# Kernel tuning notes

Measured on AMD Instinct MI355X. Metric: run time of the kernel, lower is better.

Reference implementation:

```python
import jax, jax.numpy as jnp
import numpy as np

V, E, S, B, N = 100000, 300, 1024, 64, 5
H = [512, 256, 128]

def setup_inputs() -> dict:
    key = jax.random.key(0)
    ks = jax.random.split(key, 10)
    x = jax.random.randint(ks[0], (B, S), 0, V, dtype=jnp.int32)
    # lengths must be >= n for valid n-gram counts (original assumes this)
    lengths = jax.random.randint(ks[1], (B,), N, S + 1, dtype=jnp.int32)
    sc = lambda f: 1.0 / np.sqrt(f)
    table = jax.random.normal(ks[2], (V, E), dtype=jnp.float32)
    W_slide = jax.random.uniform(ks[3], (N * E, H[0]), jnp.float32, -sc(N * E), sc(N * E))
    b_slide = jax.random.uniform(ks[4], (H[0],), jnp.float32, -sc(N * E), sc(N * E))
    W1 = jax.random.uniform(ks[5], (H[0], H[1]), jnp.float32, -sc(H[0]), sc(H[0]))
    b1 = jax.random.uniform(ks[6], (H[1],), jnp.float32, -sc(H[0]), sc(H[0]))
    W2 = jax.random.uniform(ks[7], (H[1], H[2]), jnp.float32, -sc(H[1]), sc(H[1]))
    b2 = jax.random.uniform(ks[8], (H[2],), jnp.float32, -sc(H[1]), sc(H[1]))
    return {"x": x, "lengths": lengths, "table": table, "W_slide": W_slide,
            "b_slide": b_slide, "W1": W1, "b1": b1, "W2": W2, "b2": b2}

def reference(x, lengths, table, W_slide, b_slide, W1, b1, W2, b2):
    n = N
    Wn = S - (n - 1)  # number of sliding windows per sequence
    emb = table[x]  # [B, S, E]
    # gather sliding windows: [B, Wn, n, E] -> [B, Wn, n*E]
    idx = jnp.arange(Wn)[:, None] + jnp.arange(n)[None, :]
    win = emb[:, idx].reshape(B, Wn, n * E)
    h = win @ W_slide + b_slide              # [B, Wn, H0]
    h = jax.nn.relu(h @ W1 + b1)             # [B, Wn, H1]
    h = jax.nn.relu(h @ W2 + b2)             # [B, Wn, H2]
    # ragged mean over valid n-gram positions per sample
    valid = (lengths - (n - 1)).astype(h.dtype)           # [B]
    mask = (jnp.arange(Wn)[None, :] < (lengths - (n - 1))[:, None]).astype(h.dtype)
    pooled = jnp.einsum('bwh,bw->bh', h, mask) / valid[:, None]
    return pooled
```

## Files before the change

kernel.cpp:

```cpp
#include <hip/hip_runtime.h>

#define B_N    64
#define S_LEN  1024
#define EMB    300
#define EMB_P  304
#define NGRAM  5
#define WPAD   1024
#define MTOT   (B_N * WPAD)
#define K1P    1536
#define H0     512
#define H1D    256
#define H2D    128
#define NK1    (K1P / 32)
#define NSTEP1 (K1P / 64)

#define GATHER_BLOCKS ((MTOT * (EMB_P / 4)) / 256)
#define WPREP_THREADS (H0 * K1P + H1D * H0 + H2D * H1D)
#define WPREP_BLOCKS  ((WPREP_THREADS + 255) / 256)

typedef _Float16 half8 __attribute__((ext_vector_type(8)));
typedef float  floatx4 __attribute__((ext_vector_type(4)));

typedef const __attribute__((address_space(1))) void* gptr_t;
typedef __attribute__((address_space(3))) void* sptr_t;

__device__ __forceinline__ void gload16(const void* g, void* s) {
  __builtin_amdgcn_global_load_lds((gptr_t)g, (sptr_t)s, 16, 0, 0);
}

__global__ void prep_kernel(const int* __restrict__ x,
                            const int* __restrict__ lengths,
                            const float* __restrict__ table,
                            _Float16* __restrict__ emb,
                            float* __restrict__ out,
                            const float* __restrict__ Ws,
                            const float* __restrict__ W1,
                            const float* __restrict__ W2,
                            _Float16* __restrict__ Bf1,
                            _Float16* __restrict__ Bf2,
                            _Float16* __restrict__ Bf3) {
  const int bid = blockIdx.x;
  if (bid < GATHER_BLOCKS) {
    if (bid < 32) out[bid * 256 + threadIdx.x] = 0.0f;
    const int CH = EMB_P / 4;
    int tid = bid * 256 + threadIdx.x;
    int tok = tid / CH;
    int c   = tid - tok * CH;
    int valid = lengths[tok >> 10] - (NGRAM - 1);
    int limit = ((valid + 127) & ~127) + 4;
    if ((tok & 1023) >= limit) return;
    int e   = c << 2;
    _Float16 h0, h1, h2, h3;
    if (e < EMB) {
      float4 v = *(const float4*)(table + (size_t)x[tok] * EMB + e);
      h0 = (_Float16)v.x; h1 = (_Float16)v.y; h2 = (_Float16)v.z; h3 = (_Float16)v.w;
    } else {
      h0 = h1 = h2 = h3 = (_Float16)0.0f;
    }
    union { float2 f2; _Float16 h[4]; } u;
    u.h[0] = h0; u.h[1] = h1; u.h[2] = h2; u.h[3] = h3;
    *(float2*)(emb + (size_t)tok * EMB_P + e) = u.f2;
  } else {
    int tid = (bid - GATHER_BLOCKS) * 256 + threadIdx.x;
    const int NS = H0 * K1P;
    const int N1 = H1D * H0;
    const int N2 = H2D * H1D;
    if (tid < NS) {
      int n = tid & 511, k = tid >> 9;
      float v = 0.0f;
      if (k < NGRAM * EMB_P) {
        int tn = k / EMB_P, e = k - tn * EMB_P;
        if (e < EMB) v = Ws[(size_t)(tn * EMB + e) * H0 + n];
      }
      int idx = ((((n >> 4) * NK1 + (k >> 5)) << 6) + (((k >> 3) & 3) << 4) + (n & 15)) * 8 + (k & 7);
      Bf1[idx] = (_Float16)v;
    } else if (tid < NS + N1) {
      int t = tid - NS;
      int n = t & 255, k = t >> 8;
      float v = W1[(size_t)k * H1D + n];
      int idx = ((((n >> 4) * 16 + (k >> 5)) << 6) + (((k >> 3) & 3) << 4) + (n & 15)) * 8 + (k & 7);
      Bf2[idx] = (_Float16)v;
    } else if (tid < NS + N1 + N2) {
      int t = tid - (NS + N1);
      int n = t & 127, k = t >> 7;
      float v = W2[(size_t)k * H2D + n];
      int idx = ((((n >> 4) * 8 + (k >> 5)) << 6) + (((k >> 3) & 3) << 4) + (n & 15)) * 8 + (k & 7);
      Bf3[idx] = (_Float16)v;
    }
  }
}

__global__ __launch_bounds__(256, 3)
void gemm1(const _Float16* __restrict__ A, const _Float16* __restrict__ Bf,
           const float* __restrict__ bias, _Float16* __restrict__ Cf,
           const int* __restrict__ lengths) {
  __shared__ _Float16 sA[2][128 * 64];

  const int tid  = threadIdx.x;
  const int wave = tid >> 6, lane = tid & 63;
  const int wr   = wave >> 1, wc = wave & 1;
  const int quad = lane >> 4, l16 = lane & 15;

  const int perX = gridDim.x >> 3;
  const int L  = (blockIdx.x & 7) * perX + (blockIdx.x >> 3);
  const int mt = L >> 2, nt = L & 3;
  if (((mt & 7) << 7) >= lengths[mt >> 3] - (NGRAM - 1)) return;
  const long mBase = (long)mt << 7;
  const int  nBase = nt << 7;

  const int srow0  = (wave << 3) + (lane >> 3);
  const int schunk = lane & 7;
  const _Float16* aG[4];
  int sOff[4];
#pragma unroll
  for (int p = 0; p < 4; p++) {
    int row = (p << 5) + srow0;
    int c   = schunk ^ (row & 7);
    aG[p]   = A + (mBase + row) * EMB_P + (c << 3);
    sOff[p] = (row << 6) + (schunk << 3);
  }

  const _Float16* bG[4];
#pragma unroll
  for (int j = 0; j < 4; j++)
    bG[j] = Bf + (((size_t)((nBase >> 4) + (wc << 2) + j) * NK1) << 9) + (lane << 3);

  int aOff[2][4];
#pragma unroll
  for (int s = 0; s < 2; s++)
#pragma unroll
    for (int i = 0; i < 4; i++) {
      int r    = (wr << 6) + (i << 4) + l16;
      int slot = ((s << 2) + quad) ^ (l16 & 7);
      aOff[s][i] = (r << 6) + (slot << 3);
    }

  floatx4 acc[4][4] = {};

#pragma unroll
  for (int p = 0; p < 4; p++) gload16(aG[p], &sA[0][sOff[p]]);
  half8 bCur[2][4], bNxt[2][4];
#pragma unroll
  for (int s = 0; s < 2; s++)
#pragma unroll
    for (int j = 0; j < 4; j++)
      bCur[s][j] = *(const half8*)(bG[j] + ((size_t)s << 9));

#pragma unroll 2
  for (int kk = 0; kk < NSTEP1; kk++) {
    const int cur = kk & 1;
    __syncthreads();
    if (kk + 1 < NSTEP1) {
      const int ko = (kk + 1) << 6;
#pragma unroll
      for (int p = 0; p < 4; p++) gload16(aG[p] + ko, &sA[cur ^ 1][sOff[p]]);
#pragma unroll
      for (int s = 0; s < 2; s++)
#pragma unroll
        for (int j = 0; j < 4; j++)
          bNxt[s][j] = *(const half8*)(bG[j] + (size_t)((((kk + 1) << 1) + s) << 9));
    }
#pragma unroll
    for (int s = 0; s < 2; s++) {
      half8 aFr[4];
#pragma unroll
      for (int i = 0; i < 4; i++)
        aFr[i] = *(const half8*)(&sA[cur][aOff[s][i]]);
#pragma unroll
      for (int i = 0; i < 4; i++)
#pragma unroll
        for (int j = 0; j < 4; j++)
          acc[i][j] = __builtin_amdgcn_mfma_f32_16x16x32_f16(aFr[i], bCur[s][j], acc[i][j], 0, 0, 0);
    }
#pragma unroll
    for (int s = 0; s < 2; s++)
#pragma unroll
      for (int j = 0; j < 4; j++)
        bCur[s][j] = bNxt[s][j];
  }

  __syncthreads();
  _Float16* cs = &sA[0][0];
#pragma unroll
  for (int j = 0; j < 4; j++) {
    int cl = (wc << 6) + (j << 4) + l16;
    float bv = bias[nBase + cl];
    int ksl = cl >> 5;
    int sub_hi = ((cl >> 3) & 3) << 4;
    int c7 = cl & 7;
#pragma unroll
    for (int i = 0; i < 4; i++) {
      int m16l = (wr << 2) + i;
#pragma unroll
      for (int r = 0; r < 4; r++) {
        int ml = (quad << 2) + r;
        cs[(((m16l << 2) + ksl) << 9) + ((sub_hi + ml) << 3) + c7] =
            (_Float16)(acc[i][j][r] + bv);
      }
    }
  }
  __syncthreads();
#pragma unroll
  for (int it = 0; it < 8; it++) {
    int cid = (it << 2) + wave;
    int m16l = cid >> 2, ksl = cid & 3;
    size_t g = ((size_t)(((mt << 3) + m16l) * 16 + (nt << 2) + ksl) << 9) + (lane << 3);
    *(half8*)(Cf + g) = *(const half8*)(cs + (cid << 9) + (lane << 3));
  }
}

__global__ __launch_bounds__(256, 2)
void gemm23(const _Float16* __restrict__ Af, const _Float16* __restrict__ B2,
            const _Float16* __restrict__ B3, const float* __restrict__ bias1,
            const float* __restrict__ bias2, float* __restrict__ out,
            const int* __restrict__ lengths) {
  __shared__ _Float16 sH[32768];
  __shared__ float red[2][128];

  const int tid  = threadIdx.x;
  const int wave = tid >> 6, lane = tid & 63;
  const int wr   = wave >> 1, wc = wave & 1;
  const int quad = lane >> 4, l16 = lane & 15;
  const int mt = blockIdx.x;

  const int b = mt >> 3;
  const int validw = lengths[b] - (NGRAM - 1);
  if (((mt & 7) << 7) >= validw) return;

  const _Float16* aR[4];
#pragma unroll
  for (int i = 0; i < 4; i++)
    aR[i] = Af + (((size_t)((mt << 3) + (wr << 2) + i) * 16) << 9) + (lane << 3);
  const _Float16* bR[8];
#pragma unroll
  for (int j = 0; j < 8; j++)
    bR[j] = B2 + (((size_t)((wc << 3) + j) * 16) << 9) + (lane << 3);

  floatx4 acc2[4][8] = {};
#pragma unroll 2
  for (int kk = 0; kk < 16; kk++) {
    const size_t ko = (size_t)kk << 9;
    half8 aF[4], bF[8];
#pragma unroll
    for (int i = 0; i < 4; i++) aF[i] = *(const half8*)(aR[i] + ko);
#pragma unroll
    for (int j = 0; j < 8; j++) bF[j] = *(const half8*)(bR[j] + ko);
#pragma unroll
    for (int i = 0; i < 4; i++)
#pragma unroll
      for (int j = 0; j < 8; j++)
        acc2[i][j] = __builtin_amdgcn_mfma_f32_16x16x32_f16(aF[i], bF[j], acc2[i][j], 0, 0, 0);
  }

#pragma unroll
  for (int j = 0; j < 8; j++) {
    int n = (wc << 7) + (j << 4) + l16;
    float bv = bias1[n];
    int ks = n >> 5;
    int sub_hi = ((n >> 3) & 3) << 4;
    int c7 = n & 7;
#pragma unroll
    for (int i = 0; i < 4; i++) {
      int m16l = (wr << 2) + i;
#pragma unroll
      for (int r = 0; r < 4; r++) {
        int ml = (quad << 2) + r;
        sH[(((m16l << 3) + ks) << 9) + ((sub_hi + ml) << 3) + c7] =
            (_Float16)fmaxf(acc2[i][j][r] + bv, 0.0f);
      }
    }
  }
  __syncthreads();

  const _Float16* b3R[4];
#pragma unroll
  for (int j = 0; j < 4; j++)
    b3R[j] = B3 + (((size_t)((wc << 2) + j) * 8) << 9) + (lane << 3);

  floatx4 acc3[4][4] = {};
#pragma unroll
  for (int ks = 0; ks < 8; ks++) {
    half8 aF[4], bF[4];
#pragma unroll
    for (int i = 0; i < 4; i++)
      aF[i] = *(const half8*)(sH + (((((wr << 2) + i) << 3) + ks) << 9) + (lane << 3));
#pragma unroll
    for (int j = 0; j < 4; j++) bF[j] = *(const half8*)(b3R[j] + ((size_t)ks << 9));
#pragma unroll
    for (int i = 0; i < 4; i++)
#pragma unroll
      for (int j = 0; j < 4; j++)
        acc3[i][j] = __builtin_amdgcn_mfma_f32_16x16x32_f16(aF[i], bF[j], acc3[i][j], 0, 0, 0);
  }

  float inv = 1.0f / (float)validw;
  int wBase = ((mt & 7) << 7) + (wr << 6);
#pragma unroll
  for (int j = 0; j < 4; j++) {
    int col = (wc << 6) + (j << 4) + l16;
    float bv = bias2[col];
    float p = 0.0f;
#pragma unroll
    for (int i = 0; i < 4; i++) {
#pragma unroll
      for (int r = 0; r < 4; r++) {
        int w = wBase + (i << 4) + (quad << 2) + r;
        float v = fmaxf(acc3[i][j][r] + bv, 0.0f);
        p += (w < validw) ? v : 0.0f;
      }
    }
    p *= inv;
    p += __shfl_xor(p, 16, 64);
    p += __shfl_xor(p, 32, 64);
    if (quad == 0) red[wr][col] = p;
  }
  __syncthreads();
  if (tid < 128) atomicAdd(out + b * H2D + tid, red[0][tid] + red[1][tid]);
}

extern "C" void kernel_launch(void* const* d_in, const int* in_sizes, int n_in,
                              void* d_out, int out_size, void* d_ws, size_t ws_size,
                              hipStream_t stream) {
  const int*   x       = (const int*)d_in[0];
  const int*   lengths = (const int*)d_in[1];
  const float* table   = (const float*)d_in[2];
  const float* W_slide = (const float*)d_in[3];
  const float* b_slide = (const float*)d_in[4];
  const float* W1      = (const float*)d_in[5];
  const float* b1      = (const float*)d_in[6];
  const float* W2      = (const float*)d_in[7];
  const float* b2      = (const float*)d_in[8];
  float* out = (float*)d_out;

  _Float16* ws  = (_Float16*)d_ws;
  _Float16* emb = ws;
  _Float16* Bf1 = emb + (size_t)MTOT * EMB_P + 4096;
  _Float16* Bf2 = Bf1 + (size_t)H0 * K1P;
  _Float16* Bf3 = Bf2 + (size_t)H1D * H0;
  _Float16* h1f = Bf3 + (size_t)H2D * H1D;

  prep_kernel<<<GATHER_BLOCKS + WPREP_BLOCKS, 256, 0, stream>>>(
      x, lengths, table, emb, out, W_slide, W1, W2, Bf1, Bf2, Bf3);
  gemm1<<<(MTOT / 128) * (H0 / 128), 256, 0, stream>>>(emb, Bf1, b_slide, h1f, lengths);
  gemm23<<<MTOT / 128, 256, 0, stream>>>(h1f, Bf2, Bf3, b1, b2, out, lengths);
}
```

Measured before the change: 292.3 us.

## Compact live M-tiles into a work list and widen gather stores

Adds a prep block that builds a compacted list of live 128-row tiles from the sequence lengths. gemm1 and gemm23 index that list, so live work is spread evenly across XCDs instead of leaving idle early-exit blocks scattered through the grid. The embedding gather now handles eight halves per thread with 16-byte stores. gemm23's layer-2 loop is also rewritten to double-buffer its global fragment loads in registers, which raises register pressure.

```diff
diff --git a/kernel.cpp b/kernel.cpp
--- a/kernel.cpp
+++ b/kernel.cpp
@@ -14,7 +14,7 @@
 #define NK1    (K1P / 32)
 #define NSTEP1 (K1P / 64)
 
-#define GATHER_BLOCKS ((MTOT * (EMB_P / 4)) / 256)
+#define GATHER_BLOCKS ((MTOT * 38) / 256)
 #define WPREP_THREADS (H0 * K1P + H1D * H0 + H2D * H1D)
 #define WPREP_BLOCKS  ((WPREP_THREADS + 255) / 256)
 
@@ -38,29 +38,30 @@
                             const float* __restrict__ W2,
                             _Float16* __restrict__ Bf1,
                             _Float16* __restrict__ Bf2,
-                            _Float16* __restrict__ Bf3) {
+                            _Float16* __restrict__ Bf3,
+                            int* __restrict__ meta) {
+  __shared__ int sN[64], sP[65];
   const int bid = blockIdx.x;
   if (bid < GATHER_BLOCKS) {
     if (bid < 32) out[bid * 256 + threadIdx.x] = 0.0f;
-    const int CH = EMB_P / 4;
     int tid = bid * 256 + threadIdx.x;
-    int tok = tid / CH;
-    int c   = tid - tok * CH;
+    int tok = tid / 38;
+    int c   = tid - tok * 38;
     int valid = lengths[tok >> 10] - (NGRAM - 1);
-    int limit = ((valid + 127) & ~127) + 4;
+    int limit = ((valid + 127) & ~127) + (NGRAM - 1);
     if ((tok & 1023) >= limit) return;
-    int e   = c << 2;
-    _Float16 h0, h1, h2, h3;
-    if (e < EMB) {
-      float4 v = *(const float4*)(table + (size_t)x[tok] * EMB + e);
-      h0 = (_Float16)v.x; h1 = (_Float16)v.y; h2 = (_Float16)v.z; h3 = (_Float16)v.w;
-    } else {
-      h0 = h1 = h2 = h3 = (_Float16)0.0f;
-    }
-    union { float2 f2; _Float16 h[4]; } u;
-    u.h[0] = h0; u.h[1] = h1; u.h[2] = h2; u.h[3] = h3;
-    *(float2*)(emb + (size_t)tok * EMB_P + e) = u.f2;
-  } else {
+    int e = c << 3;
+    const float* row = table + (size_t)x[tok] * EMB + e;
+    float4 v0 = *(const float4*)row;
+    float4 v1 = make_float4(0.0f, 0.0f, 0.0f, 0.0f);
+    if (e + 4 < EMB) v1 = *(const float4*)(row + 4);
+    union { half8 h8; _Float16 h[8]; } u;
+    u.h[0] = (_Float16)v0.x; u.h[1] = (_Float16)v0.y;
+    u.h[2] = (_Float16)v0.z; u.h[3] = (_Float16)v0.w;
+    u.h[4] = (_Float16)v1.x; u.h[5] = (_Float16)v1.y;
+    u.h[6] = (_Float16)v1.z; u.h[7] = (_Float16)v1.w;
+    *(half8*)(emb + (size_t)tok * EMB_P + e) = u.h8;
+  } else if (bid < GATHER_BLOCKS + WPREP_BLOCKS) {
     int tid = (bid - GATHER_BLOCKS) * 256 + threadIdx.x;
     const int NS = H0 * K1P;
     const int N1 = H1D * H0;
@@ -87,24 +88,42 @@
       int idx = ((((n >> 4) * 8 + (k >> 5)) << 6) + (((k >> 3) & 3) << 4) + (n & 15)) * 8 + (k & 7);
       Bf3[idx] = (_Float16)v;
     }
+  } else {
+    int t = threadIdx.x;
+    if (t < 64) sN[t] = (lengths[t] - (NGRAM - 1) + 127) >> 7;
+    __syncthreads();
+    if (t == 0) {
+      int s = 0;
+      for (int i = 0; i < 64; i++) { sP[i] = s; s += sN[i]; }
+      sP[64] = s;
+      meta[0] = s;
+    }
+    __syncthreads();
+    if (t < 64) {
+      int base = sP[t], n = sN[t];
+      for (int i = 0; i < n; i++) meta[8 + base + i] = (t << 3) + i;
+    }
   }
 }
 
 __global__ __launch_bounds__(256, 3)
 void gemm1(const _Float16* __restrict__ A, const _Float16* __restrict__ Bf,
            const float* __restrict__ bias, _Float16* __restrict__ Cf,
-           const int* __restrict__ lengths) {
+           const int* __restrict__ meta) {
   __shared__ _Float16 sA[2][128 * 64];
+
+  const int nLive4 = meta[0] << 2;
+  const int xcd = blockIdx.x & 7, bi = blockIdx.x >> 3;
+  const int q = nLive4 >> 3, r = nLive4 & 7;
+  if (bi >= q + (xcd < r ? 1 : 0)) return;
+  const int L = xcd * q + (xcd < r ? xcd : r) + bi;
+  const int mt = meta[8 + (L >> 2)], nt = L & 3;
 
   const int tid  = threadIdx.x;
   const int wave = tid >> 6, lane = tid & 63;
   const int wr   = wave >> 1, wc = wave & 1;
   const int quad = lane >> 4, l16 = lane & 15;
 
-  const int perX = gridDim.x >> 3;
-  const int L  = (blockIdx.x & 7) * perX + (blockIdx.x >> 3);
-  const int mt = L >> 2, nt = L & 3;
-  if (((mt & 7) << 7) >= lengths[mt >> 3] - (NGRAM - 1)) return;
   const long mBase = (long)mt << 7;
   const int  nBase = nt << 7;
 
@@ -130,9 +149,9 @@
   for (int s = 0; s < 2; s++)
 #pragma unroll
     for (int i = 0; i < 4; i++) {
-      int r    = (wr << 6) + (i << 4) + l16;
+      int rr   = (wr << 6) + (i << 4) + l16;
       int slot = ((s << 2) + quad) ^ (l16 & 7);
-      aOff[s][i] = (r << 6) + (slot << 3);
+      aOff[s][i] = (rr << 6) + (slot << 3);
     }
 
   floatx4 acc[4][4] = {};
@@ -192,10 +211,10 @@
     for (int i = 0; i < 4; i++) {
       int m16l = (wr << 2) + i;
 #pragma unroll
-      for (int r = 0; r < 4; r++) {
-        int ml = (quad << 2) + r;
+      for (int rr = 0; rr < 4; rr++) {
+        int ml = (quad << 2) + rr;
         cs[(((m16l << 2) + ksl) << 9) + ((sub_hi + ml) << 3) + c7] =
-            (_Float16)(acc[i][j][r] + bv);
+            (_Float16)(acc[i][j][rr] + bv);
       }
     }
   }
@@ -213,43 +232,52 @@
 void gemm23(const _Float16* __restrict__ Af, const _Float16* __restrict__ B2,
             const _Float16* __restrict__ B3, const float* __restrict__ bias1,
             const float* __restrict__ bias2, float* __restrict__ out,
-            const int* __restrict__ lengths) {
+            const int* __restrict__ lengths, const int* __restrict__ meta) {
   __shared__ _Float16 sH[32768];
   __shared__ float red[2][128];
+
+  if ((int)blockIdx.x >= meta[0]) return;
+  const int mt = meta[8 + blockIdx.x];
 
   const int tid  = threadIdx.x;
   const int wave = tid >> 6, lane = tid & 63;
   const int wr   = wave >> 1, wc = wave & 1;
   const int quad = lane >> 4, l16 = lane & 15;
-  const int mt = blockIdx.x;
 
   const int b = mt >> 3;
   const int validw = lengths[b] - (NGRAM - 1);
-  if (((mt & 7) << 7) >= validw) return;
-
-  const _Float16* aR[4];
-#pragma unroll
-  for (int i = 0; i < 4; i++)
-    aR[i] = Af + (((size_t)((mt << 3) + (wr << 2) + i) * 16) << 9) + (lane << 3);
-  const _Float16* bR[8];
-#pragma unroll
-  for (int j = 0; j < 8; j++)
-    bR[j] = B2 + (((size_t)((wc << 3) + j) * 16) << 9) + (lane << 3);
+
+  const _Float16* aB = Af + (((size_t)((mt << 3) + (wr << 2)) * 16) << 9) + (lane << 3);
+  const _Float16* bB = B2 + ((size_t)wc << 16) + (lane << 3);
 
   floatx4 acc2[4][8] = {};
-#pragma unroll 2
-  for (int kk = 0; kk < 16; kk++) {
-    const size_t ko = (size_t)kk << 9;
-    half8 aF[4], bF[8];
-#pragma unroll
-    for (int i = 0; i < 4; i++) aF[i] = *(const half8*)(aR[i] + ko);
-#pragma unroll
-    for (int j = 0; j < 8; j++) bF[j] = *(const half8*)(bR[j] + ko);
+  half8 aP[4], bP[8], aQ[4], bQ[8];
+
+  auto loadA = [&](half8* d, int kk) {
+#pragma unroll
+    for (int i = 0; i < 4; i++)
+      d[i] = *(const half8*)(aB + ((size_t)kk << 9) + ((size_t)i << 13));
+  };
+  auto loadB = [&](half8* d, int kk) {
+#pragma unroll
+    for (int j = 0; j < 8; j++)
+      d[j] = *(const half8*)(bB + ((size_t)kk << 9) + ((size_t)j << 13));
+  };
+  auto mfmaStep = [&](const half8* aF, const half8* bF) {
 #pragma unroll
     for (int i = 0; i < 4; i++)
 #pragma unroll
       for (int j = 0; j < 8; j++)
         acc2[i][j] = __builtin_amdgcn_mfma_f32_16x16x32_f16(aF[i], bF[j], acc2[i][j], 0, 0, 0);
+  };
+
+  loadA(aP, 0); loadB(bP, 0);
+#pragma unroll
+  for (int kk = 0; kk < 16; kk += 2) {
+    loadA(aQ, kk + 1); loadB(bQ, kk + 1);
+    mfmaStep(aP, bP);
+    if (kk + 2 < 16) { loadA(aP, kk + 2); loadB(bP, kk + 2); }
+    mfmaStep(aQ, bQ);
   }
 
 #pragma unroll
@@ -263,10 +291,10 @@
     for (int i = 0; i < 4; i++) {
       int m16l = (wr << 2) + i;
 #pragma unroll
-      for (int r = 0; r < 4; r++) {
-        int ml = (quad << 2) + r;
+      for (int rr = 0; rr < 4; rr++) {
+        int ml = (quad << 2) + rr;
         sH[(((m16l << 3) + ks) << 9) + ((sub_hi + ml) << 3) + c7] =
-            (_Float16)fmaxf(acc2[i][j][r] + bv, 0.0f);
+            (_Float16)fmaxf(acc2[i][j][rr] + bv, 0.0f);
       }
     }
   }
@@ -303,9 +331,9 @@
 #pragma unroll
     for (int i = 0; i < 4; i++) {
 #pragma unroll
-      for (int r = 0; r < 4; r++) {
-        int w = wBase + (i << 4) + (quad << 2) + r;
-        float v = fmaxf(acc3[i][j][r] + bv, 0.0f);
+      for (int rr = 0; rr < 4; rr++) {
+        int w = wBase + (i << 4) + (quad << 2) + rr;
+        float v = fmaxf(acc3[i][j][rr] + bv, 0.0f);
         p += (w < validw) ? v : 0.0f;
       }
     }
@@ -338,9 +366,10 @@
   _Float16* Bf2 = Bf1 + (size_t)H0 * K1P;
   _Float16* Bf3 = Bf2 + (size_t)H1D * H0;
   _Float16* h1f = Bf3 + (size_t)H2D * H1D;
-
-  prep_kernel<<<GATHER_BLOCKS + WPREP_BLOCKS, 256, 0, stream>>>(
-      x, lengths, table, emb, out, W_slide, W1, W2, Bf1, Bf2, Bf3);
-  gemm1<<<(MTOT / 128) * (H0 / 128), 256, 0, stream>>>(emb, Bf1, b_slide, h1f, lengths);
-  gemm23<<<MTOT / 128, 256, 0, stream>>>(h1f, Bf2, Bf3, b1, b2, out, lengths);
-}
+  int*      meta = (int*)(h1f + (size_t)MTOT * H0);
+
+  prep_kernel<<<GATHER_BLOCKS + WPREP_BLOCKS + 1, 256, 0, stream>>>(
+      x, lengths, table, emb, out, W_slide, W1, W2, Bf1, Bf2, Bf3, meta);
+  gemm1<<<(MTOT / 128) * (H0 / 128), 256, 0, stream>>>(emb, Bf1, b_slide, h1f, meta);
+  gemm23<<<MTOT / 128, 256, 0, stream>>>(h1f, Bf2, Bf3, b1, b2, out, lengths, meta);
+}
```

Result: faster. 276.3 us (-5.5%).
